# Optimization experiments

Measured on AMD Instinct MI355X. Metric: run time of the kernel, lower is better.

Reference implementation:

```python
import jax, jax.numpy as jnp
import numpy as np

TEMPERATURE = 0.1

def _l2norm(x):
    return x / jnp.linalg.norm(x, axis=-1, keepdims=True)

def setup_inputs() -> dict:
    key = jax.random.key(0)
    k1, k2, k3 = jax.random.split(key, 3)
    N_AUG, B, F, Q = 2, 256, 128, 65536
    V = _l2norm(jax.random.normal(k1, (N_AUG, B, F), dtype=jnp.float32))
    L = _l2norm(jax.random.normal(k2, (B, F), dtype=jnp.float32))
    queue = _l2norm(jax.random.normal(k3, (Q, F), dtype=jnp.float32))
    return {"V": V, "L": L, "queue": queue}

def reference(V, L, queue):
    # V: (J, B, F), L: (B, F), queue: (Q, F)
    J, B, F = V.shape
    inv_t = 1.0 / TEMPERATURE
    # pos[j, b] = V[j, b] . L[b] / T  (diagonal batch pairings)
    pos = jnp.einsum('jbf,bf->jb', V, L) * inv_t                 # (J, B)
    # qlog[j, b, q] = V[j, b] . queue[q] / T
    qlog = jnp.einsum('jbf,qf->jbq', V, queue) * inv_t           # (J, B, Q)
    # Original: denom[j,b] = log( sum_i exp(pos[j,i]) + sum_q exp(qlog[j,b,q]) )
    # == logsumexp over the concatenation of pos[j,:] and qlog[j,b,:].
    bat = jnp.broadcast_to(pos[:, None, :], (J, B, B))           # (J, B, B)
    combined = jnp.concatenate([bat, qlog], axis=-1)             # (J, B, B+Q)
    denom = jax.nn.logsumexp(combined, axis=-1)                  # (J, B)
    # loss = -(1/B) * sum_{b} sum_{j} (pos[j,b] - denom[j,b])
    loss = -jnp.sum(pos - denom) / B
    return loss
```

## Files before the change

### kernel.cpp

```cpp
#include <hip/hip_runtime.h>


typedef float  float4v __attribute__((ext_vector_type(4)));
typedef short  short8  __attribute__((ext_vector_type(8)));

#define AS1 __attribute__((address_space(1)))
#define AS3 __attribute__((address_space(3)))

__device__ __forceinline__ unsigned short f2bf(float f) {
    union { float f; unsigned u; } v; v.f = f;
    unsigned r = v.u + 0x7FFFu + ((v.u >> 16) & 1u);
    return (unsigned short)(r >> 16);
}


__global__ __launch_bounds__(256) void convert_prep_kernel(
        const float* __restrict__ V, const float* __restrict__ L,
        const float* __restrict__ Qf,
        unsigned short* __restrict__ qbf, unsigned short* __restrict__ abf,
        float* __restrict__ pos) {
    const int tid = threadIdx.x;
    const int gt  = blockIdx.x * 256 + tid;
    const float4* q4 = (const float4*)Qf;
    uint2* qo = (uint2*)qbf;
    #pragma unroll
    for (int i = 0; i < 4; ++i) {
        const int g = i * 524288 + gt;
        const float4 q = q4[g];
        uint2 p;
        p.x = (unsigned)f2bf(q.x) | ((unsigned)f2bf(q.y) << 16);
        p.y = (unsigned)f2bf(q.z) | ((unsigned)f2bf(q.w) << 16);
        qo[g] = p;
    }
    if (blockIdx.x < 64) {
        const float4 v = ((const float4*)V)[gt];
        uint2 p;
        p.x = (unsigned)f2bf(v.x) | ((unsigned)f2bf(v.y) << 16);
        p.y = (unsigned)f2bf(v.z) | ((unsigned)f2bf(v.w) << 16);
        ((uint2*)abf)[gt] = p;
    } else if (blockIdx.x < 128) {
        const int blk  = blockIdx.x - 64;
        const int w    = tid >> 6;
        const int lane = tid & 63;
        #pragma unroll
        for (int i = 0; i < 2; ++i) {
            const int r = blk * 8 + w * 2 + i;
            const int b = r & 255;
            const float2 v = *reinterpret_cast<const float2*>(V + r * 128 + lane * 2);
            const float2 l = *reinterpret_cast<const float2*>(L + b * 128 + lane * 2);
            float p = v.x * l.x + v.y * l.y;
            #pragma unroll
            for (int off = 32; off; off >>= 1) p += __shfl_xor(p, off);
            if (lane == 0) pos[r] = 10.0f * p;
        }
    }
}

__global__ __launch_bounds__(256, 2) void gemm_exp_kernel(
        const unsigned short* __restrict__ abf,
        const unsigned short* __restrict__ qbf,
        float* __restrict__ gbuf) {
    __shared__ unsigned short Bs[2][64 * 128];
    __shared__ float rowsum[256];

    const int tid  = threadIdx.x;
    const int bid  = blockIdx.x;
    const int mt   = bid >> 8;
    const int ng   = bid & 255;
    const int m0   = mt * 256;
    const int nb   = ng * 256;

    const int w    = tid >> 6;
    const int lane = tid & 63;
    const int quad = lane >> 4;
    const int l16  = lane & 15;
    const int wrow = w * 64;

    short8 a[4][4];
    #pragma unroll
    for (int mi = 0; mi < 4; ++mi)
        #pragma unroll
        for (int kk = 0; kk < 4; ++kk)
            a[mi][kk] = *(const short8*)&abf[(m0 + wrow + mi * 16 + l16) * 128
                                             + (kk * 4 + quad) * 8];

    auto issueB = [&](int t) {
        unsigned short* buf = &Bs[t & 1][0];
        const unsigned short* base = qbf + (nb + t * 64) * 128;
        #pragma unroll
        for (int r = 0; r < 4; ++r) {
            const int slot = r * 256 + w * 64 + lane;
            const int row  = slot >> 4;
            const int c    = (slot & 15) ^ (row & 15);
            __builtin_amdgcn_global_load_lds((AS1 void*)(base + row * 128 + c * 8),
                (AS3 void*)&buf[(r * 256 + w * 64) * 8], 16, 0, 0);
        }
    };
    issueB(0);
    issueB(1);

    float rs[4][4];
    #pragma unroll
    for (int mi = 0; mi < 4; ++mi)
        #pragma unroll
        for (int r = 0; r < 4; ++r) rs[mi][r] = 0.0f;

    #pragma unroll 1
    for (int t = 0; t < 4; ++t) {
        if (t < 3) __builtin_amdgcn_s_waitcnt(0x0F74);
        else       __builtin_amdgcn_s_waitcnt(0x0F70);
        __builtin_amdgcn_s_barrier();
        const unsigned short* buf = &Bs[t & 1][0];

        float4v acc[4][4];
        #pragma unroll
        for (int mi = 0; mi < 4; ++mi)
            #pragma unroll
            for (int ni = 0; ni < 4; ++ni)
                acc[mi][ni] = (float4v){0.f, 0.f, 0.f, 0.f};

        #pragma unroll
        for (int kk = 0; kk < 4; ++kk) {
            const int c = kk * 4 + quad;
            short8 b[4];
            #pragma unroll
            for (int ni = 0; ni < 4; ++ni) {
                const int row = ni * 16 + l16;
                b[ni] = *(const short8*)&buf[row * 128 + ((c ^ (row & 15)) << 3)];
            }
            #pragma unroll
            for (int mi = 0; mi < 4; ++mi)
                #pragma unroll
                for (int ni = 0; ni < 4; ++ni)
                    acc[mi][ni] = __builtin_amdgcn_mfma_f32_16x16x32_bf16(
                        a[mi][kk], b[ni], acc[mi][ni], 0, 0, 0);
        }

        #pragma unroll
        for (int mi = 0; mi < 4; ++mi)
            #pragma unroll
            for (int ni = 0; ni < 4; ++ni)
                #pragma unroll
                for (int r = 0; r < 4; ++r)
                    rs[mi][r] += exp2f(acc[mi][ni][r] * 14.426950408889634f);

        if (t < 2) {
            __builtin_amdgcn_s_barrier();
            issueB(t + 2);
        }
    }

    #pragma unroll
    for (int mi = 0; mi < 4; ++mi)
        #pragma unroll
        for (int r = 0; r < 4; ++r) {
            float v = rs[mi][r];
            v += __shfl_xor(v, 1);
            v += __shfl_xor(v, 2);
            v += __shfl_xor(v, 4);
            v += __shfl_xor(v, 8);
            if (l16 == 0) rowsum[wrow + mi * 16 + quad * 4 + r] = v;
        }
    __syncthreads();
    gbuf[(m0 + tid) * 256 + ng] = rowsum[tid];
}

__global__ __launch_bounds__(1024) void finalize_fused_kernel(
        const float* __restrict__ pos,
        const float* __restrict__ gbuf,
        float* __restrict__ out) {
    __shared__ float wsum[16];
    __shared__ float Sp[2];
    const int tid  = threadIdx.x;
    const int w    = tid >> 6;
    const int lane = tid & 63;

    float e = (tid < 512) ? __expf(pos[tid]) : 0.0f;
    #pragma unroll
    for (int off = 32; off; off >>= 1) e += __shfl_xor(e, off);
    if (lane == 0) wsum[w] = e;
    __syncthreads();
    if (tid == 0) {
        Sp[0] = wsum[0] + wsum[1] + wsum[2] + wsum[3];
        Sp[1] = wsum[4] + wsum[5] + wsum[6] + wsum[7];
    }
    __syncthreads();

    const int r = tid >> 1;
    const int h = tid & 1;
    const float4* g = (const float4*)(gbuf + r * 256 + h * 128);
    float s = 0.0f;
    #pragma unroll
    for (int i = 0; i < 32; ++i) {
        const float4 v = g[i];
        s += (v.x + v.y) + (v.z + v.w);
    }
    s += __shfl_xor(s, 1);

    float contrib = 0.0f;
    if (h == 0) contrib = pos[r] - __logf(Sp[r >> 8] + s);
    #pragma unroll
    for (int off = 32; off; off >>= 1) contrib += __shfl_xor(contrib, off);
    __syncthreads();
    if (lane == 0) wsum[w] = contrib;
    __syncthreads();
    if (tid == 0) {
        float tot = 0.0f;
        #pragma unroll
        for (int i = 0; i < 16; ++i) tot += wsum[i];
        out[0] = -tot / 256.0f;
    }
}


__global__ void prep_kernel(const float* __restrict__ V,
                            const float* __restrict__ L,
                            float* __restrict__ pos,
                            float* __restrict__ Sq) {
    const int blk  = blockIdx.x;
    const int tid  = threadIdx.x;
    if (tid < 8) Sq[blk * 8 + tid] = 0.0f;
    const int w    = tid >> 6;
    const int lane = tid & 63;
    #pragma unroll
    for (int i = 0; i < 2; ++i) {
        const int r = blk * 8 + w * 2 + i;
        const int b = r & 255;
        const float2 v = *reinterpret_cast<const float2*>(V + r * 128 + lane * 2);
        const float2 l = *reinterpret_cast<const float2*>(L + b * 128 + lane * 2);
        float p = v.x * l.x + v.y * l.y;
        #pragma unroll
        for (int off = 32; off; off >>= 1) p += __shfl_xor(p, off);
        if (lane == 0) pos[r] = 10.0f * p;
    }
}

__global__ __launch_bounds__(256) void gemm_exp_fallback(
        const float* __restrict__ V,
        const float* __restrict__ Q,
        float* __restrict__ Sq) {
    __shared__ unsigned short As[128 * 128];
    __shared__ unsigned short Bs[128 * 128];
    const int tid = threadIdx.x;
    const int m0  = blockIdx.y * 128;
    const int n0  = blockIdx.x * 128;
    #pragma unroll
    for (int i = 0; i < 16; ++i) {
        const int idx = i * 256 + tid;
        const int row = idx >> 5;
        const int c4  = idx & 31;
        const float4 a = *reinterpret_cast<const float4*>(V + (m0 + row) * 128 + c4 * 4);
        const float4 b = *reinterpret_cast<const float4*>(Q + (n0 + row) * 128 + c4 * 4);
        const int chunk = ((c4 >> 1) ^ (row & 15));
        const int off   = row * 128 + (chunk << 3) + ((c4 & 1) << 2);
        const uint2 pa = make_uint2((unsigned)f2bf(a.x) | ((unsigned)f2bf(a.y) << 16),
                                    (unsigned)f2bf(a.z) | ((unsigned)f2bf(a.w) << 16));
        const uint2 pb = make_uint2((unsigned)f2bf(b.x) | ((unsigned)f2bf(b.y) << 16),
                                    (unsigned)f2bf(b.z) | ((unsigned)f2bf(b.w) << 16));
        *reinterpret_cast<uint2*>(&As[off]) = pa;
        *reinterpret_cast<uint2*>(&Bs[off]) = pb;
    }
    __syncthreads();
    const int w    = tid >> 6;
    const int lane = tid & 63;
    const int quad = lane >> 4;
    const int l16  = lane & 15;
    const int wrow = (w >> 1) * 64;
    const int wcol = (w & 1) * 64;
    float4v acc[4][4];
    #pragma unroll
    for (int mi = 0; mi < 4; ++mi)
        #pragma unroll
        for (int ni = 0; ni < 4; ++ni)
            acc[mi][ni] = (float4v){0.f, 0.f, 0.f, 0.f};
    #pragma unroll
    for (int kk = 0; kk < 4; ++kk) {
        const int kchunk = kk * 4 + quad;
        short8 a[4], b[4];
        #pragma unroll
        for (int mi = 0; mi < 4; ++mi) {
            const int row = wrow + mi * 16 + l16;
            a[mi] = *reinterpret_cast<const short8*>(&As[row * 128 + ((kchunk ^ (row & 15)) << 3)]);
        }
        #pragma unroll
        for (int ni = 0; ni < 4; ++ni) {
            const int row = wcol + ni * 16 + l16;
            b[ni] = *reinterpret_cast<const short8*>(&Bs[row * 128 + ((kchunk ^ (row & 15)) << 3)]);
        }
        #pragma unroll
        for (int mi = 0; mi < 4; ++mi)
            #pragma unroll
            for (int ni = 0; ni < 4; ++ni)
                acc[mi][ni] = __builtin_amdgcn_mfma_f32_16x16x32_bf16(a[mi], b[ni], acc[mi][ni], 0, 0, 0);
    }
    __syncthreads();
    float* rowsum = reinterpret_cast<float*>(As);
    #pragma unroll
    for (int mi = 0; mi < 4; ++mi) {
        float rsv[4] = {0.f, 0.f, 0.f, 0.f};
        #pragma unroll
        for (int ni = 0; ni < 4; ++ni)
            #pragma unroll
            for (int r = 0; r < 4; ++r)
                rsv[r] += __expf(10.0f * acc[mi][ni][r]);
        #pragma unroll
        for (int r = 0; r < 4; ++r) {
            float vsum = rsv[r];
            vsum += __shfl_xor(vsum, 1);
            vsum += __shfl_xor(vsum, 2);
            vsum += __shfl_xor(vsum, 4);
            vsum += __shfl_xor(vsum, 8);
            if (l16 == 0)
                rowsum[(w & 1) * 128 + wrow + mi * 16 + quad * 4 + r] = vsum;
        }
    }
    __syncthreads();
    if (tid < 128)
        atomicAdd(&Sq[m0 + tid], rowsum[tid] + rowsum[128 + tid]);
}

__global__ void finalize_kernel(const float* __restrict__ pos,
                                const float* __restrict__ Sq,
                                float* __restrict__ out) {
    __shared__ float wsum[8];
    __shared__ float Sp[2];
    const int tid  = threadIdx.x;
    const int w    = tid >> 6;
    const int lane = tid & 63;
    const float p = pos[tid];
    float e = __expf(p);
    #pragma unroll
    for (int off = 32; off; off >>= 1) e += __shfl_xor(e, off);
    if (lane == 0) wsum[w] = e;
    __syncthreads();
    if (tid == 0) {
        Sp[0] = wsum[0] + wsum[1] + wsum[2] + wsum[3];
        Sp[1] = wsum[4] + wsum[5] + wsum[6] + wsum[7];
    }
    __syncthreads();
    const int j = tid >> 8;
    float contrib = p - __logf(Sp[j] + Sq[tid]);
    #pragma unroll
    for (int off = 32; off; off >>= 1) contrib += __shfl_xor(contrib, off);
    if (lane == 0) wsum[w] = contrib;
    __syncthreads();
    if (tid == 0) {
        float tot = 0.f;
        #pragma unroll
        for (int i = 0; i < 8; ++i) tot += wsum[i];
        out[0] = -tot / 256.0f;
    }
}


extern "C" void kernel_launch(void* const* d_in, const int* in_sizes, int n_in,
                              void* d_out, int out_size, void* d_ws, size_t ws_size,
                              hipStream_t stream) {
    const float* V     = (const float*)d_in[0];
    const float* L     = (const float*)d_in[1];
    const float* queue = (const float*)d_in[2];
    float* out = (float*)d_out;

    const size_t need = (size_t)65536 * 128 * 2 + (size_t)512 * 128 * 2
                      + 512 * 4 + (size_t)512 * 256 * 4;
    if (ws_size >= need) {
        unsigned short* qbf = (unsigned short*)d_ws;
        unsigned short* abf = qbf + (size_t)65536 * 128;
        float* pos  = (float*)(abf + 512 * 128);
        float* gbuf = pos + 512;
        convert_prep_kernel<<<2048, 256, 0, stream>>>(V, L, queue, qbf, abf, pos);
        gemm_exp_kernel<<<512, 256, 0, stream>>>(abf, qbf, gbuf);
        finalize_fused_kernel<<<1, 1024, 0, stream>>>(pos, gbuf, out);
    } else {
        float* pos = (float*)d_ws;
        float* Sq  = pos + 512;
        prep_kernel<<<64, 256, 0, stream>>>(V, L, pos, Sq);
        dim3 grid(512, 4);
        gemm_exp_fallback<<<grid, 256, 0, stream>>>(V, queue, Sq);
        finalize_kernel<<<1, 512, 0, stream>>>(pos, Sq, out);
    }
}
```

Baseline: 118.3 us.

## Fuse queue bf16 conversion into GEMM and stage each queue tile once

Drops the separate pass that converted the whole queue to bf16 in global memory. Each GEMM block now loads a 128-row queue tile as fp32, converts it to bf16 into swizzled LDS once, then loops over both 256-row M tiles, so every queue row is read exactly once. This removes the write and re-read of the bf16 queue copy, at the cost of losing the async double-buffered LDS loads and adding a small extra reduction kernel over the per-block partial sums.

```diff
diff --git a/kernel.cpp b/kernel.cpp
--- a/kernel.cpp
+++ b/kernel.cpp
@@ -3,9 +3,6 @@
 
 typedef float  float4v __attribute__((ext_vector_type(4)));
 typedef short  short8  __attribute__((ext_vector_type(8)));
-
-#define AS1 __attribute__((address_space(1)))
-#define AS3 __attribute__((address_space(3)))
 
 __device__ __forceinline__ unsigned short f2bf(float f) {
     union { float f; unsigned u; } v; v.f = f;
@@ -14,31 +11,18 @@
 }
 
 
-__global__ __launch_bounds__(256) void convert_prep_kernel(
+__global__ __launch_bounds__(256) void prep2_kernel(
         const float* __restrict__ V, const float* __restrict__ L,
-        const float* __restrict__ Qf,
-        unsigned short* __restrict__ qbf, unsigned short* __restrict__ abf,
-        float* __restrict__ pos) {
+        unsigned short* __restrict__ abf, float* __restrict__ pos) {
     const int tid = threadIdx.x;
-    const int gt  = blockIdx.x * 256 + tid;
-    const float4* q4 = (const float4*)Qf;
-    uint2* qo = (uint2*)qbf;
-    #pragma unroll
-    for (int i = 0; i < 4; ++i) {
-        const int g = i * 524288 + gt;
-        const float4 q = q4[g];
-        uint2 p;
-        p.x = (unsigned)f2bf(q.x) | ((unsigned)f2bf(q.y) << 16);
-        p.y = (unsigned)f2bf(q.z) | ((unsigned)f2bf(q.w) << 16);
-        qo[g] = p;
-    }
     if (blockIdx.x < 64) {
+        const int gt = blockIdx.x * 256 + tid;
         const float4 v = ((const float4*)V)[gt];
         uint2 p;
         p.x = (unsigned)f2bf(v.x) | ((unsigned)f2bf(v.y) << 16);
         p.y = (unsigned)f2bf(v.z) | ((unsigned)f2bf(v.w) << 16);
         ((uint2*)abf)[gt] = p;
-    } else if (blockIdx.x < 128) {
+    } else {
         const int blk  = blockIdx.x - 64;
         const int w    = tid >> 6;
         const int lane = tid & 63;
@@ -56,19 +40,16 @@
     }
 }
 
-__global__ __launch_bounds__(256, 2) void gemm_exp_kernel(
+__global__ __launch_bounds__(256, 2) void gemm_exp_fused_kernel(
         const unsigned short* __restrict__ abf,
-        const unsigned short* __restrict__ qbf,
+        const float* __restrict__ Qf,
         float* __restrict__ gbuf) {
-    __shared__ unsigned short Bs[2][64 * 128];
+    __shared__ unsigned short Bs[128 * 128];
     __shared__ float rowsum[256];
 
     const int tid  = threadIdx.x;
     const int bid  = blockIdx.x;
-    const int mt   = bid >> 8;
-    const int ng   = bid & 255;
-    const int m0   = mt * 256;
-    const int nb   = ng * 256;
+    const int nb   = bid * 128;
 
     const int w    = tid >> 6;
     const int lane = tid & 63;
@@ -76,98 +57,105 @@
     const int l16  = lane & 15;
     const int wrow = w * 64;
 
-    short8 a[4][4];
-    #pragma unroll
-    for (int mi = 0; mi < 4; ++mi)
-        #pragma unroll
-        for (int kk = 0; kk < 4; ++kk)
-            a[mi][kk] = *(const short8*)&abf[(m0 + wrow + mi * 16 + l16) * 128
-                                             + (kk * 4 + quad) * 8];
-
-    auto issueB = [&](int t) {
-        unsigned short* buf = &Bs[t & 1][0];
-        const unsigned short* base = qbf + (nb + t * 64) * 128;
-        #pragma unroll
-        for (int r = 0; r < 4; ++r) {
-            const int slot = r * 256 + w * 64 + lane;
-            const int row  = slot >> 4;
-            const int c    = (slot & 15) ^ (row & 15);
-            __builtin_amdgcn_global_load_lds((AS1 void*)(base + row * 128 + c * 8),
-                (AS3 void*)&buf[(r * 256 + w * 64) * 8], 16, 0, 0);
-        }
-    };
-    issueB(0);
-    issueB(1);
-
-    float rs[4][4];
-    #pragma unroll
-    for (int mi = 0; mi < 4; ++mi)
-        #pragma unroll
-        for (int r = 0; r < 4; ++r) rs[mi][r] = 0.0f;
+    #pragma unroll
+    for (int i = 0; i < 16; ++i) {
+        const int idx = i * 256 + tid;
+        const int row = idx >> 5;
+        const int c4  = idx & 31;
+        const float4 q = *reinterpret_cast<const float4*>(Qf + (nb + row) * 128 + c4 * 4);
+        uint2 p;
+        p.x = (unsigned)f2bf(q.x) | ((unsigned)f2bf(q.y) << 16);
+        p.y = (unsigned)f2bf(q.z) | ((unsigned)f2bf(q.w) << 16);
+        const int chunk = (c4 >> 1) ^ (row & 15);
+        *reinterpret_cast<uint2*>(&Bs[row * 128 + (chunk << 3) + ((c4 & 1) << 2)]) = p;
+    }
+    __syncthreads();
 
     #pragma unroll 1
-    for (int t = 0; t < 4; ++t) {
-        if (t < 3) __builtin_amdgcn_s_waitcnt(0x0F74);
-        else       __builtin_amdgcn_s_waitcnt(0x0F70);
-        __builtin_amdgcn_s_barrier();
-        const unsigned short* buf = &Bs[t & 1][0];
-
-        float4v acc[4][4];
+    for (int mt = 0; mt < 2; ++mt) {
+        const int m0 = mt * 256;
+
+        short8 a[4][4];
         #pragma unroll
         for (int mi = 0; mi < 4; ++mi)
             #pragma unroll
-            for (int ni = 0; ni < 4; ++ni)
-                acc[mi][ni] = (float4v){0.f, 0.f, 0.f, 0.f};
-
-        #pragma unroll
-        for (int kk = 0; kk < 4; ++kk) {
-            const int c = kk * 4 + quad;
-            short8 b[4];
-            #pragma unroll
-            for (int ni = 0; ni < 4; ++ni) {
-                const int row = ni * 16 + l16;
-                b[ni] = *(const short8*)&buf[row * 128 + ((c ^ (row & 15)) << 3)];
-            }
+            for (int kk = 0; kk < 4; ++kk)
+                a[mi][kk] = *(const short8*)&abf[(m0 + wrow + mi * 16 + l16) * 128
+                                                 + (kk * 4 + quad) * 8];
+
+        float rs[4][4];
+        #pragma unroll
+        for (int mi = 0; mi < 4; ++mi)
+            #pragma unroll
+            for (int r = 0; r < 4; ++r) rs[mi][r] = 0.0f;
+
+        #pragma unroll
+        for (int sub = 0; sub < 2; ++sub) {
+            float4v acc[4][4];
             #pragma unroll
             for (int mi = 0; mi < 4; ++mi)
                 #pragma unroll
                 for (int ni = 0; ni < 4; ++ni)
-                    acc[mi][ni] = __builtin_amdgcn_mfma_f32_16x16x32_bf16(
-                        a[mi][kk], b[ni], acc[mi][ni], 0, 0, 0);
+                    acc[mi][ni] = (float4v){0.f, 0.f, 0.f, 0.f};
+
+            #pragma unroll
+            for (int kk = 0; kk < 4; ++kk) {
+                const int c = kk * 4 + quad;
+                short8 b[4];
+                #pragma unroll
+                for (int ni = 0; ni < 4; ++ni) {
+                    const int row = sub * 64 + ni * 16 + l16;
+                    b[ni] = *(const short8*)&Bs[row * 128 + ((c ^ (row & 15)) << 3)];
+                }
+                #pragma unroll
+                for (int mi = 0; mi < 4; ++mi)
+                    #pragma unroll
+                    for (int ni = 0; ni < 4; ++ni)
+                        acc[mi][ni] = __builtin_amdgcn_mfma_f32_16x16x32_bf16(
+                            a[mi][kk], b[ni], acc[mi][ni], 0, 0, 0);
+            }
+
+            #pragma unroll
+            for (int mi = 0; mi < 4; ++mi)
+                #pragma unroll
+                for (int ni = 0; ni < 4; ++ni)
+                    #pragma unroll
+                    for (int r = 0; r < 4; ++r)
+                        rs[mi][r] += exp2f(acc[mi][ni][r] * 14.426950408889634f);
         }
 
         #pragma unroll
         for (int mi = 0; mi < 4; ++mi)
             #pragma unroll
-            for (int ni = 0; ni < 4; ++ni)
-                #pragma unroll
-                for (int r = 0; r < 4; ++r)
-                    rs[mi][r] += exp2f(acc[mi][ni][r] * 14.426950408889634f);
-
-        if (t < 2) {
-            __builtin_amdgcn_s_barrier();
-            issueB(t + 2);
-        }
-    }
-
-    #pragma unroll
-    for (int mi = 0; mi < 4; ++mi)
-        #pragma unroll
-        for (int r = 0; r < 4; ++r) {
-            float v = rs[mi][r];
-            v += __shfl_xor(v, 1);
-            v += __shfl_xor(v, 2);
-            v += __shfl_xor(v, 4);
-            v += __shfl_xor(v, 8);
-            if (l16 == 0) rowsum[wrow + mi * 16 + quad * 4 + r] = v;
-        }
-    __syncthreads();
-    gbuf[(m0 + tid) * 256 + ng] = rowsum[tid];
+            for (int r = 0; r < 4; ++r) {
+                float v = rs[mi][r];
+                v += __shfl_xor(v, 1);
+                v += __shfl_xor(v, 2);
+                v += __shfl_xor(v, 4);
+                v += __shfl_xor(v, 8);
+                if (l16 == 0) rowsum[wrow + mi * 16 + quad * 4 + r] = v;
+            }
+        __syncthreads();
+        gbuf[bid * 512 + mt * 256 + tid] = rowsum[tid];
+        __syncthreads();
+    }
+}
+
+__global__ __launch_bounds__(256) void reduce_k_kernel(
+        const float* __restrict__ gbuf, float* __restrict__ gbuf2) {
+    const int g = blockIdx.x * 256 + threadIdx.x;
+    const int m = g & 511;
+    const int s = g >> 9;
+    float acc = 0.0f;
+    #pragma unroll
+    for (int k = 0; k < 16; ++k)
+        acc += gbuf[(s * 16 + k) * 512 + m];
+    gbuf2[s * 512 + m] = acc;
 }
 
 __global__ __launch_bounds__(1024) void finalize_fused_kernel(
         const float* __restrict__ pos,
-        const float* __restrict__ gbuf,
+        const float* __restrict__ gbuf2,
         float* __restrict__ out) {
     __shared__ float wsum[16];
     __shared__ float Sp[2];
@@ -186,19 +174,16 @@
     }
     __syncthreads();
 
-    const int r = tid >> 1;
+    const int m = tid >> 1;
     const int h = tid & 1;
-    const float4* g = (const float4*)(gbuf + r * 256 + h * 128);
     float s = 0.0f;
     #pragma unroll
-    for (int i = 0; i < 32; ++i) {
-        const float4 v = g[i];
-        s += (v.x + v.y) + (v.z + v.w);
-    }
+    for (int k = 0; k < 16; ++k)
+        s += gbuf2[(h * 16 + k) * 512 + m];
     s += __shfl_xor(s, 1);
 
     float contrib = 0.0f;
-    if (h == 0) contrib = pos[r] - __logf(Sp[r >> 8] + s);
+    if (h == 0) contrib = pos[m] - __logf(Sp[m >> 8] + s);
     #pragma unroll
     for (int off = 32; off; off >>= 1) contrib += __shfl_xor(contrib, off);
     __syncthreads();
@@ -361,16 +346,17 @@
     const float* queue = (const float*)d_in[2];
     float* out = (float*)d_out;
 
-    const size_t need = (size_t)65536 * 128 * 2 + (size_t)512 * 128 * 2
-                      + 512 * 4 + (size_t)512 * 256 * 4;
+    const size_t need = (size_t)512 * 128 * 2 + 512 * 4
+                      + (size_t)512 * 512 * 4 + (size_t)32 * 512 * 4;
     if (ws_size >= need) {
-        unsigned short* qbf = (unsigned short*)d_ws;
-        unsigned short* abf = qbf + (size_t)65536 * 128;
-        float* pos  = (float*)(abf + 512 * 128);
-        float* gbuf = pos + 512;
-        convert_prep_kernel<<<2048, 256, 0, stream>>>(V, L, queue, qbf, abf, pos);
-        gemm_exp_kernel<<<512, 256, 0, stream>>>(abf, qbf, gbuf);
-        finalize_fused_kernel<<<1, 1024, 0, stream>>>(pos, gbuf, out);
+        unsigned short* abf = (unsigned short*)d_ws;
+        float* pos   = (float*)(abf + 512 * 128);
+        float* gbuf  = pos + 512;
+        float* gbuf2 = gbuf + (size_t)512 * 512;
+        prep2_kernel<<<128, 256, 0, stream>>>(V, L, abf, pos);
+        gemm_exp_fused_kernel<<<512, 256, 0, stream>>>(abf, queue, gbuf);
+        reduce_k_kernel<<<64, 256, 0, stream>>>(gbuf, gbuf2);
+        finalize_fused_kernel<<<1, 1024, 0, stream>>>(pos, gbuf2, out);
     } else {
         float* pos = (float*)d_ws;
         float* Sq  = pos + 512;
```

Measured after the change: 102.8 us. -13.1%, faster.
